# Kernel optimization log

Measured on AMD Instinct MI355X. Metric: run time of the kernel, lower is better.

The kernel has to match this reference:

```python
import jax, jax.numpy as jnp
import numpy as np

N_BINS = 64
N_SPLINE_DIMS = 3 * N_BINS - 1
N_GENES = 5000
N_GENES_OI = 5000
N_CUTS = 500_000
WINDOW_A, WINDOW_B = -10000.0, 10000.0
AB = WINDOW_B - WINDOW_A
MIN_BIN_WIDTH = 1e-3
MIN_BIN_HEIGHT = 1e-3
MIN_DERIVATIVE = 1e-3
# default init so that softplus(init) + min_derivative == 1 at the tails
DEFAULT_INIT = float(np.log(np.exp(1.0 - MIN_DERIVATIVE) - 1.0))
LOG_HALF = float(np.log(0.5))
LOG_AB = float(np.log(AB))


def setup_inputs() -> dict:
    key = jax.random.key(0)
    k1, k2, k3, k4 = jax.random.split(key, 4)
    value = jax.random.uniform(k1, (N_CUTS,), minval=WINDOW_A, maxval=WINDOW_B, dtype=jnp.float32)
    delta_spline = jax.random.normal(k2, (N_CUTS, N_SPLINE_DIMS), dtype=jnp.float32) * 0.1
    genes_oi = jax.random.randint(k3, (N_GENES_OI,), 0, N_GENES, dtype=jnp.int64 if jax.config.jax_enable_x64 else jnp.int32)
    local_gene_ix = jax.random.randint(k4, (N_CUTS,), 0, N_GENES_OI, dtype=jnp.int64 if jax.config.jax_enable_x64 else jnp.int32)
    spline_weight = jnp.full((N_GENES, N_SPLINE_DIMS), DEFAULT_INIT, dtype=jnp.float32)
    return {"value": value, "delta_spline": delta_spline, "genes_oi": genes_oi,
            "local_gene_ix": local_gene_ix, "spline_weight": spline_weight}


def _rqs_inverse(x, uw, uh, ud_padded):
    """Rational-quadratic spline, inverse pass, domain [-1,1]x[-1,1].
    x: (N,1); uw, uh: (N,1,K); ud_padded: (N,1,K+1)."""
    K = uw.shape[-1]
    pad = [(0, 0)] * (uw.ndim - 1) + [(1, 0)]

    w = jax.nn.softmax(uw, axis=-1)
    w = MIN_BIN_WIDTH + (1.0 - MIN_BIN_WIDTH * K) * w
    cw = jnp.pad(jnp.cumsum(w, axis=-1), pad)
    cw = 2.0 * cw - 1.0  # map [0,1] -> [-1,1]
    cw = cw.at[..., 0].set(-1.0).at[..., -1].set(1.0)
    w = cw[..., 1:] - cw[..., :-1]

    d = MIN_DERIVATIVE + jax.nn.softplus(ud_padded)  # (N,1,K+1)

    h = jax.nn.softmax(uh, axis=-1)
    h = MIN_BIN_HEIGHT + (1.0 - MIN_BIN_HEIGHT * K) * h
    ch = jnp.pad(jnp.cumsum(h, axis=-1), pad)
    ch = 2.0 * ch - 1.0
    ch = ch.at[..., 0].set(-1.0).at[..., -1].set(1.0)
    h = ch[..., 1:] - ch[..., :-1]

    # searchsorted over cumulative heights (inverse pass)
    bins = ch.at[..., -1].add(1e-6)
    idx = jnp.clip(jnp.sum((x[..., None] >= bins).astype(jnp.int32), axis=-1) - 1, 0, K - 1)

    def gather(t):
        return jnp.take_along_axis(t, idx[..., None], axis=-1)[..., 0]

    in_cw = gather(cw)
    in_w = gather(w)
    in_ch = gather(ch)
    in_h = gather(h)
    delta = gather(h / w)
    d0 = gather(d)
    d1 = jnp.take_along_axis(d, (idx + 1)[..., None], axis=-1)[..., 0]

    dy = x - in_ch
    s = d0 + d1 - 2.0 * delta
    a = dy * s + in_h * (delta - d0)
    b = in_h * d0 - dy * s
    c = -delta * dy
    disc = b * b - 4.0 * a * c
    root = (2.0 * c) / (-b - jnp.sqrt(jnp.maximum(disc, 0.0)))  # theta in [0,1]
    y = root * in_w + in_cw

    tom = root * (1.0 - root)
    denom = delta + s * tom
    deriv_num = (delta * delta) * (d1 * root * root + 2.0 * delta * tom + d0 * (1.0 - root) * (1.0 - root))
    logabsdet = -(jnp.log(deriv_num) - 2.0 * jnp.log(denom))  # negated for inverse
    return y, logabsdet


def reference(value, delta_spline, genes_oi, local_gene_ix, spline_weight):
    K = N_BINS
    spline = spline_weight[genes_oi][local_gene_ix] + delta_spline  # (N, 3K-1)
    uw = spline[:, None, :K]           # (N,1,K)
    uh = spline[:, None, K:2 * K]      # (N,1,K)
    ud = spline[:, None, 2 * K:]       # (N,1,K-1)

    x = (((value - WINDOW_A) / AB) - 0.5) * 2.0  # normalize to [-1,1]
    x = x[:, None]  # (N,1)

    inside = (x >= -1.0) & (x <= 1.0)
    ud_padded = jnp.pad(ud, [(0, 0), (0, 0), (1, 1)], constant_values=DEFAULT_INIT)
    xc = jnp.clip(x, -1.0, 1.0)
    _, logdet = _rqs_inverse(xc, uw, uh, ud_padded)
    logdet = jnp.where(inside, logdet, 0.0)  # linear tails: logabsdet = 0
    return LOG_HALF + logdet - LOG_AB  # (N,1)
```

## Files before the change

kernel.cpp:

```cpp
#include <hip/hip_runtime.h>

#define NSPL 191
constexpr float MIN_W = 0.001f, MIN_H = 0.001f, MIN_D = 0.001f;
constexpr float W_A = -10000.0f, AB = 20000.0f;
constexpr float LOG_HALF = -0.69314718055994530942f;
constexpr float LOG_AB   = 9.90348755253612804622f;

#define CPB 256
#define TC  32
#define PITCH 33

__global__ __launch_bounds__(CPB, 3) void rqs_tpc_kernel(
    const float* __restrict__ value,
    const float* __restrict__ dsg,
    const int*   __restrict__ genes_oi,
    const int*   __restrict__ lgi,
    const float* __restrict__ sw,
    float* __restrict__ out, int n)
{
    __shared__ float tile[CPB * PITCH];

    const int t  = threadIdx.x;
    const int i0 = blockIdx.x * CPB;
    const int i  = i0 + t;
    const int ic = min(i, n - 1);

    const int g = genes_oi[lgi[ic]];
    const float* __restrict__ swr = sw  + (long)g  * NSPL;
    const float* __restrict__ dsr = dsg + (long)ic * NSPL;

    const float v = value[ic];
    float x = fmaf(v - W_A, 2.0f / AB, -1.0f);
    const bool inside = (x >= -1.0f) && (x <= 1.0f);
    x = fminf(fmaxf(x, -1.0f), 1.0f);

    float eh[64];
    float s0 = 0.f, s1 = 0.f, s2a = 0.f, s3 = 0.f;
    float h0 = 0.f, h1 = 0.f, h2a = 0.f, h3 = 0.f;

    const int c  = t & (TC - 1);
    const int r0 = t >> 5;

    #pragma unroll
    for (int tt = 0; tt < 4; ++tt) {
        const int jc = tt * TC;

        float tmp[32];
        #pragma unroll
        for (int rr = 0; rr < 32; ++rr) {
            const int r  = r0 + (rr << 3);
            const int rg = min(i0 + r, n - 1);
            tmp[rr] = dsg[(long)rg * NSPL + jc + c];
        }
        #pragma unroll
        for (int rr = 0; rr < 32; ++rr) {
            const int r = r0 + (rr << 3);
            tile[r * PITCH + c] = tmp[rr];
        }
        __syncthreads();

        #pragma unroll
        for (int j = 0; j < TC; ++j) {
            const float u = tile[t * PITCH + j] + swr[jc + j];
            const float e = __expf(u);
            if (tt < 2) {
                if ((j & 3) == 0) s0 += e;
                else if ((j & 3) == 1) s1 += e;
                else if ((j & 3) == 2) s2a += e;
                else s3 += e;
            } else {
                eh[jc + j - 64] = e;
                if ((j & 3) == 0) h0 += e;
                else if ((j & 3) == 1) h1 += e;
                else if ((j & 3) == 2) h2a += e;
                else h3 += e;
            }
        }
        __syncthreads();
    }

    const float Sw = (s0 + s1) + (s2a + s3);
    const float Sh = (h0 + h1) + (h2a + h3);
    const float wsc2 = 2.0f * __fdividef(1.0f - MIN_W * 64.0f, Sw);
    const float hsc2 = 2.0f * __fdividef(1.0f - MIN_H * 64.0f, Sh);

    float Eh = 0.0f, capEh = 0.0f;
    int idx = 0;
    #pragma unroll
    for (int j = 0; j < 63; ++j) {
        Eh += eh[j];
        const float chr = fmaf(hsc2, Eh, 2.0f * MIN_H * (float)(j + 1) - 1.0f);
        const bool take = (x >= chr);
        idx  += take ? 1 : 0;
        capEh = take ? Eh : capEh;
    }

    const float ew_i = __expf(dsr[idx]      + swr[idx]);
    const float eh_i = __expf(dsr[64 + idx] + swr[64 + idx]);
    const int c0 = 127 + max(idx, 1);
    const int c1 = 128 + min(idx, 62);
    const float u0 = dsr[c0] + swr[c0];
    const float u1 = dsr[c1] + swr[c1];
    const float d0 = (idx == 0)  ? 1.0f : (MIN_D + __logf(1.0f + __expf(u0)));
    const float d1 = (idx == 63) ? 1.0f : (MIN_D + __logf(1.0f + __expf(u1)));

    const float in_w = fmaf(wsc2, ew_i, 2.0f * MIN_W);
    const float in_h = fmaf(hsc2, eh_i, 2.0f * MIN_H);
    const float ch_l = fmaf(hsc2, capEh, fmaf(2.0f * MIN_H, (float)idx, -1.0f));

    const float delta = __fdividef(in_h, in_w);
    const float dy = x - ch_l;
    const float ss = d0 + d1 - 2.0f * delta;
    const float aa = dy * ss + in_h * (delta - d0);
    const float bb = in_h * d0 - dy * ss;
    const float cc = -delta * dy;
    const float disc = bb * bb - 4.0f * aa * cc;
    const float root = __fdividef(2.0f * cc, -bb - sqrtf(fmaxf(disc, 0.0f)));
    const float tom = root * (1.0f - root);
    const float denom = delta + ss * tom;
    const float omr = 1.0f - root;
    const float dnum = delta * delta * (d1 * root * root + 2.0f * delta * tom + d0 * omr * omr);
    const float logabsdet = -(__logf(dnum) - 2.0f * __logf(denom));

    if (i < n)
        out[i] = LOG_HALF + (inside ? logabsdet : 0.0f) - LOG_AB;
}

extern "C" void kernel_launch(void* const* d_in, const int* in_sizes, int n_in,
                              void* d_out, int out_size, void* d_ws, size_t ws_size,
                              hipStream_t stream) {
    const float* value         = (const float*)d_in[0];
    const float* delta_spline  = (const float*)d_in[1];
    const int*   genes_oi      = (const int*)d_in[2];
    const int*   local_gene_ix = (const int*)d_in[3];
    const float* spline_weight = (const float*)d_in[4];
    float* out = (float*)d_out;

    const int n = in_sizes[0];
    const int blocks = (n + CPB - 1) / CPB;
    rqs_tpc_kernel<<<blocks, CPB, 0, stream>>>(
        value, delta_spline, genes_oi, local_gene_ix, spline_weight, out, n);
}
```

Baseline: 585.7 us.

## Process each cut with a 16-lane group using cross-lane scans and reductions

Replaces the one-thread-per-cut design, which staged the delta_spline rows through a transposed shared-memory tile, with 16 lanes per cut. Each lane loads four width and four height logits as vectors, and the softmax sums, the prefix sum over heights and the bin count are done with DPP and ds_swizzle cross-lane operations. ds_bpermute then fetches the cumulative height at the chosen bin. This drops the shared-memory staging, the block barriers and the serial 63-step search, at the cost of running 16 times more threads that do redundant scalar work and loading misaligned float4 vectors from rows of 191 floats.

```diff
diff --git a/kernel.cpp b/kernel.cpp
--- a/kernel.cpp
+++ b/kernel.cpp
@@ -6,107 +6,110 @@
 constexpr float LOG_HALF = -0.69314718055994530942f;
 constexpr float LOG_AB   = 9.90348755253612804622f;
 
-#define CPB 256
-#define TC  32
-#define PITCH 33
+typedef float f4 __attribute__((ext_vector_type(4), aligned(4)));
 
-__global__ __launch_bounds__(CPB, 3) void rqs_tpc_kernel(
+template<int CTRL>
+__device__ __forceinline__ float dpp_add(float x) {
+    int t = __builtin_amdgcn_update_dpp(0, __float_as_int(x), CTRL, 0xf, 0xf, true);
+    return x + __int_as_float(t);
+}
+template<int PAT>
+__device__ __forceinline__ float swz_f(float x) {
+    return __int_as_float(__builtin_amdgcn_ds_swizzle(__float_as_int(x), PAT));
+}
+template<int PAT>
+__device__ __forceinline__ int swz_i(int x) {
+    return __builtin_amdgcn_ds_swizzle(x, PAT);
+}
+
+__global__ __launch_bounds__(256, 4) void rqs_g16_kernel(
     const float* __restrict__ value,
     const float* __restrict__ dsg,
     const int*   __restrict__ genes_oi,
     const int*   __restrict__ lgi,
-    const float* __restrict__ sw,
+    const float* __restrict__ swg,
     float* __restrict__ out, int n)
 {
-    __shared__ float tile[CPB * PITCH];
-
-    const int t  = threadIdx.x;
-    const int i0 = blockIdx.x * CPB;
-    const int i  = i0 + t;
-    const int ic = min(i, n - 1);
+    const int lane = threadIdx.x & 63;
+    const int sub  = lane & 15;
+    const int grp  = lane >> 4;
+    const int wv   = threadIdx.x >> 6;
+    const long ii  = (long)blockIdx.x * 16 + wv * 4 + grp;
+    const int  ic  = (int)(ii < (long)n ? ii : (long)(n - 1));
 
     const int g = genes_oi[lgi[ic]];
-    const float* __restrict__ swr = sw  + (long)g  * NSPL;
+    const float v = value[ic];
+
     const float* __restrict__ dsr = dsg + (long)ic * NSPL;
+    const float* __restrict__ swr = swg + (long)g  * NSPL;
 
-    const float v = value[ic];
+    const int cb = 4 * sub;
+    const f4 dw = *(const f4*)(dsr + cb);
+    const f4 dh = *(const f4*)(dsr + 64 + cb);
+    const f4 ww = *(const f4*)(swr + cb);
+    const f4 wh = *(const f4*)(swr + 64 + cb);
+
     float x = fmaf(v - W_A, 2.0f / AB, -1.0f);
     const bool inside = (x >= -1.0f) && (x <= 1.0f);
     x = fminf(fmaxf(x, -1.0f), 1.0f);
 
-    float eh[64];
-    float s0 = 0.f, s1 = 0.f, s2a = 0.f, s3 = 0.f;
-    float h0 = 0.f, h1 = 0.f, h2a = 0.f, h3 = 0.f;
+    const float ew0 = __expf(dw.x + ww.x), ew1 = __expf(dw.y + ww.y);
+    const float ew2 = __expf(dw.z + ww.z), ew3 = __expf(dw.w + ww.w);
+    const float eh0 = __expf(dh.x + wh.x), eh1 = __expf(dh.y + wh.y);
+    const float eh2 = __expf(dh.z + wh.z), eh3 = __expf(dh.w + wh.w);
 
-    const int c  = t & (TC - 1);
-    const int r0 = t >> 5;
+    float Sw = (ew0 + ew1) + (ew2 + ew3);
+    Sw += swz_f<0x041F>(Sw); Sw += swz_f<0x081F>(Sw);
+    Sw += swz_f<0x101F>(Sw); Sw += swz_f<0x201F>(Sw);
 
-    #pragma unroll
-    for (int tt = 0; tt < 4; ++tt) {
-        const int jc = tt * TC;
+    float c0 = eh0, c1 = c0 + eh1, c2 = c1 + eh2, c3 = c2 + eh3;
+    float t = c3;
+    t = dpp_add<0x111>(t);
+    t = dpp_add<0x112>(t);
+    t = dpp_add<0x114>(t);
+    t = dpp_add<0x118>(t);
+    const float base = t - c3;
+    c0 += base; c1 += base; c2 += base; c3 += base;
+    const float Sh = swz_f<0x1F0>(c3);
 
-        float tmp[32];
-        #pragma unroll
-        for (int rr = 0; rr < 32; ++rr) {
-            const int r  = r0 + (rr << 3);
-            const int rg = min(i0 + r, n - 1);
-            tmp[rr] = dsg[(long)rg * NSPL + jc + c];
-        }
-        #pragma unroll
-        for (int rr = 0; rr < 32; ++rr) {
-            const int r = r0 + (rr << 3);
-            tile[r * PITCH + c] = tmp[rr];
-        }
-        __syncthreads();
+    const float wsc2 = __fdividef(2.0f * (1.0f - 64.0f * MIN_W), Sw);
+    const float hsc2 = __fdividef(2.0f * (1.0f - 64.0f * MIN_H), Sh);
 
-        #pragma unroll
-        for (int j = 0; j < TC; ++j) {
-            const float u = tile[t * PITCH + j] + swr[jc + j];
-            const float e = __expf(u);
-            if (tt < 2) {
-                if ((j & 3) == 0) s0 += e;
-                else if ((j & 3) == 1) s1 += e;
-                else if ((j & 3) == 2) s2a += e;
-                else s3 += e;
-            } else {
-                eh[jc + j - 64] = e;
-                if ((j & 3) == 0) h0 += e;
-                else if ((j & 3) == 1) h1 += e;
-                else if ((j & 3) == 2) h2a += e;
-                else h3 += e;
-            }
-        }
-        __syncthreads();
-    }
+    const float off2 = 2.0f * MIN_H;
+    const float p1 = (float)(cb + 1);
+    const float e0v = fmaf(hsc2, c0, fmaf(off2, p1,          -1.0f));
+    const float e1v = fmaf(hsc2, c1, fmaf(off2, p1 + 1.0f,   -1.0f));
+    const float e2v = fmaf(hsc2, c2, fmaf(off2, p1 + 2.0f,   -1.0f));
+    float       e3v = fmaf(hsc2, c3, fmaf(off2, p1 + 3.0f,   -1.0f));
+    if (sub == 15) e3v = 2.0f;
+    int cnt = (x >= e0v) + (x >= e1v) + (x >= e2v) + (x >= e3v);
+    cnt += swz_i<0x041F>(cnt); cnt += swz_i<0x081F>(cnt);
+    cnt += swz_i<0x101F>(cnt); cnt += swz_i<0x201F>(cnt);
+    const int idx = cnt;
 
-    const float Sw = (s0 + s1) + (s2a + s3);
-    const float Sh = (h0 + h1) + (h2a + h3);
-    const float wsc2 = 2.0f * __fdividef(1.0f - MIN_W * 64.0f, Sw);
-    const float hsc2 = 2.0f * __fdividef(1.0f - MIN_H * 64.0f, Sh);
-
-    float Eh = 0.0f, capEh = 0.0f;
-    int idx = 0;
-    #pragma unroll
-    for (int j = 0; j < 63; ++j) {
-        Eh += eh[j];
-        const float chr = fmaf(hsc2, Eh, 2.0f * MIN_H * (float)(j + 1) - 1.0f);
-        const bool take = (x >= chr);
-        idx  += take ? 1 : 0;
-        capEh = take ? Eh : capEh;
-    }
+    const int j  = idx - 1;
+    const int q  = (j >> 2) & 15;
+    const int ad = (grp * 16 + q) << 2;
+    const float g0 = __int_as_float(__builtin_amdgcn_ds_bpermute(ad, __float_as_int(c0)));
+    const float g1 = __int_as_float(__builtin_amdgcn_ds_bpermute(ad, __float_as_int(c1)));
+    const float g2 = __int_as_float(__builtin_amdgcn_ds_bpermute(ad, __float_as_int(c2)));
+    const float g3 = __int_as_float(__builtin_amdgcn_ds_bpermute(ad, __float_as_int(c3)));
+    const int r = j & 3;
+    float sel = (r == 0) ? g0 : (r == 1) ? g1 : (r == 2) ? g2 : g3;
+    const float capEh = (idx == 0) ? 0.0f : sel;
 
     const float ew_i = __expf(dsr[idx]      + swr[idx]);
     const float eh_i = __expf(dsr[64 + idx] + swr[64 + idx]);
-    const int c0 = 127 + max(idx, 1);
-    const int c1 = 128 + min(idx, 62);
-    const float u0 = dsr[c0] + swr[c0];
-    const float u1 = dsr[c1] + swr[c1];
+    const int cd0 = 127 + (idx > 1 ? idx : 1);
+    const int cd1 = 128 + (idx < 62 ? idx : 62);
+    const float u0 = dsr[cd0] + swr[cd0];
+    const float u1 = dsr[cd1] + swr[cd1];
     const float d0 = (idx == 0)  ? 1.0f : (MIN_D + __logf(1.0f + __expf(u0)));
     const float d1 = (idx == 63) ? 1.0f : (MIN_D + __logf(1.0f + __expf(u1)));
 
     const float in_w = fmaf(wsc2, ew_i, 2.0f * MIN_W);
     const float in_h = fmaf(hsc2, eh_i, 2.0f * MIN_H);
-    const float ch_l = fmaf(hsc2, capEh, fmaf(2.0f * MIN_H, (float)idx, -1.0f));
+    const float ch_l = fmaf(hsc2, capEh, fmaf(off2, (float)idx, -1.0f));
 
     const float delta = __fdividef(in_h, in_w);
     const float dy = x - ch_l;
@@ -122,8 +125,8 @@
     const float dnum = delta * delta * (d1 * root * root + 2.0f * delta * tom + d0 * omr * omr);
     const float logabsdet = -(__logf(dnum) - 2.0f * __logf(denom));
 
-    if (i < n)
-        out[i] = LOG_HALF + (inside ? logabsdet : 0.0f) - LOG_AB;
+    if (sub == 0 && ii < (long)n)
+        out[ii] = LOG_HALF + (inside ? logabsdet : 0.0f) - LOG_AB;
 }
 
 extern "C" void kernel_launch(void* const* d_in, const int* in_sizes, int n_in,
@@ -137,7 +140,8 @@
     float* out = (float*)d_out;
 
     const int n = in_sizes[0];
-    const int blocks = (n + CPB - 1) / CPB;
-    rqs_tpc_kernel<<<blocks, CPB, 0, stream>>>(
+    const int cuts_per_block = 16;
+    const int blocks = (n + cuts_per_block - 1) / cuts_per_block;
+    rqs_g16_kernel<<<blocks, 256, 0, stream>>>(
         value, delta_spline, genes_oi, local_gene_ix, spline_weight, out, n);
 }
```

Result: faster. 501.0 us (-14.5%).
